# Performance work log

Hardware: AMD Instinct MI355X
Metric: run time of the kernel (lower is better)

Reference implementation:

```python
import jax, jax.numpy as jnp
import numpy as np


def setup_inputs() -> dict:
    key = jax.random.key(0)
    k1, k2, k3 = jax.random.split(key, 3)
    B, IN, H, OUT = 2048, 4096, 4096, 1024
    x = jax.random.normal(k1, (B, IN), dtype=jnp.float32)
    fc1_weight = jax.random.randint(k2, (H, IN), 0, 2).astype(jnp.int32)
    fc2_weight = jax.random.randint(k3, (OUT, H), 0, 2).astype(jnp.int32)
    return {"x": x, "fc1_weight": fc1_weight, "fc2_weight": fc2_weight, "threshold": 2048}


def _binary_popcount_matmul(a, w):
    # a: (B, K) in {0,1}, w: (N, K) in {0,1}
    # matches = sum_k 1 - (a XOR w) = a@w.T + (1-a)@(1-w).T  (identical math,
    # avoids materializing the (B, N, K) XNOR tensor the naive code builds)
    return jnp.einsum('bk,nk->bn', a, w) + jnp.einsum('bk,nk->bn', 1 - a, 1 - w)


def reference(x, fc1_weight, fc2_weight, threshold):
    xb = (x.reshape(x.shape[0], -1) >= 0).astype(jnp.int32)   # binarize input
    pc1 = _binary_popcount_matmul(xb, fc1_weight)              # (B, H) popcounts
    act1 = (pc1 >= threshold).astype(jnp.int32)                # threshold activation
    pc2 = _binary_popcount_matmul(act1, fc2_weight)            # (B, OUT) popcounts
    return pc2
```

## Files before the change

### kernel.cpp

```cpp
#include <hip/hip_runtime.h>
#include <stdint.h>

typedef int v4i  __attribute__((ext_vector_type(4)));
typedef int v16i __attribute__((ext_vector_type(16)));

__device__ __forceinline__ void gload_lds16(const void* g, void* l) {
    __builtin_amdgcn_global_load_lds(
        (const __attribute__((address_space(1))) void*)g,
        (__attribute__((address_space(3))) void*)l, 16, 0, 0);
}

template<typename T, bool ISFLOAT>
__global__ __launch_bounds__(512)
void pack_frag(const T* __restrict__ in, int8_t* __restrict__ F, int K) {
    __shared__ int8_t lbuf[32 * 528];
    const int t  = threadIdx.x;
    const int db = blockIdx.y;
    const int c0 = blockIdx.x << 9;

    #pragma unroll
    for (int p = 0; p < 8; ++p) {
        int idx = p * 512 + t;
        int row = idx >> 7, c4 = idx & 127;
        uint32_t b;
        if constexpr (ISFLOAT) {
            const float4 v = *(const float4*)(in + (size_t)(db * 32 + row) * K + c0 + c4 * 4);
            b =  (v.x >= 0.0f ? 0x01u : 0xFFu)
              | ((v.y >= 0.0f ? 0x01u : 0xFFu) << 8)
              | ((v.z >= 0.0f ? 0x01u : 0xFFu) << 16)
              | ((v.w >= 0.0f ? 0x01u : 0xFFu) << 24);
        } else {
            const int4 v = *(const int4*)(in + (size_t)(db * 32 + row) * K + c0 + c4 * 4);
            b =  (v.x ? 0x01u : 0xFFu)
              | ((v.y ? 0x01u : 0xFFu) << 8)
              | ((v.z ? 0x01u : 0xFFu) << 16)
              | ((v.w ? 0x01u : 0xFFu) << 24);
        }
        *(uint32_t*)(lbuf + row * 528 + c4 * 4) = b;
    }
    __syncthreads();

    const int s  = t >> 5;
    const int l0 = t & 31;
    const int KC = K >> 5;
    int8_t* dst = F + ((size_t)db * KC + (c0 >> 5) + s) * 1024;
    uint4 v0 = *(const uint4*)(lbuf + l0 * 528 + s * 32);
    uint4 v1 = *(const uint4*)(lbuf + l0 * 528 + s * 32 + 16);
    *(uint4*)(dst + l0 * 16) = v0;
    *(uint4*)(dst + (l0 + 32) * 16) = v1;
}

__global__ __launch_bounds__(512, 1)
void bnn_l1_opt(const int8_t* __restrict__ Af,
                const int8_t* __restrict__ Bf,
                const int* __restrict__ thr_ptr,
                int8_t* __restrict__ actf)
{
    constexpr int KC  = 128;
    constexpr int NKT = 64;
    constexpr uint32_t BUFSZ = 24576;

    __shared__ int8_t lds[4 * 24576];

    const int tid  = threadIdx.x;
    const int lane = tid & 63;
    const int wv   = tid >> 6;
    const int wr   = wv >> 2, wc = wv & 3;

    const int g   = blockIdx.x;
    const int idx = g >> 3;
    const int bn  = (g & 7) * 2 + (idx >> 4);
    const int bm  = idx & 15;

    const int8_t* gsrc[3];
    uint32_t loff[3];
    #pragma unroll
    for (int c = 0; c < 3; ++c) {
        int s = c * 512 + tid;
        if (s < 512) {
            int R = s >> 7, kk = (s >> 6) & 1, ln = s & 63;
            gsrc[c] = Af + ((size_t)(bm * 4 + R) * KC + kk) * 1024 + ln * 16;
            loff[c] = (uint32_t)s * 16;
        } else {
            int s2 = s - 512;
            int Cb = s2 >> 7, kk = (s2 >> 6) & 1, ln = s2 & 63;
            gsrc[c] = Bf + ((size_t)(bn * 8 + Cb) * KC + kk) * 1024 + ln * 16;
            loff[c] = 8192u + (uint32_t)s2 * 16;
        }
    }

    auto issue3 = [&](uint32_t bufo) {
        gload_lds16(gsrc[0], lds + bufo + loff[0]); gsrc[0] += 2048;
        gload_lds16(gsrc[1], lds + bufo + loff[1]); gsrc[1] += 2048;
        gload_lds16(gsrc[2], lds + bufo + loff[2]); gsrc[2] += 2048;
    };

    v16i acc[2][2];
    #pragma unroll
    for (int i = 0; i < 2; ++i)
        #pragma unroll
        for (int j = 0; j < 2; ++j) acc[i][j] = {};

    issue3(0);
    issue3(BUFSZ);
    issue3(2 * BUFSZ);

#define KT_BODY(KT, P)                                                         \
    {                                                                          \
        const int kt_ = (KT);                                                  \
        if (kt_ < NKT - 2)       asm volatile("s_waitcnt vmcnt(6)" ::: "memory"); \
        else if (kt_ == NKT - 2) asm volatile("s_waitcnt vmcnt(3)" ::: "memory"); \
        else                     asm volatile("s_waitcnt vmcnt(0)" ::: "memory"); \
        __builtin_amdgcn_sched_barrier(0);                                     \
        __builtin_amdgcn_s_barrier();                                          \
        __builtin_amdgcn_sched_barrier(0);                                     \
        const int8_t* Ab = lds + (P) * 24576 + wr * 4096 + lane * 16;          \
        const int8_t* Bb = lds + (P) * 24576 + 8192 + wc * 4096 + lane * 16;   \
        v4i a00 = *(const v4i*)(Ab + 0);                                       \
        v4i a01 = *(const v4i*)(Ab + 1024);                                    \
        v4i a10 = *(const v4i*)(Ab + 2048);                                    \
        v4i a11 = *(const v4i*)(Ab + 3072);                                    \
        v4i b00 = *(const v4i*)(Bb + 0);                                       \
        v4i b01 = *(const v4i*)(Bb + 1024);                                    \
        v4i b10 = *(const v4i*)(Bb + 2048);                                    \
        v4i b11 = *(const v4i*)(Bb + 3072);                                    \
        if (kt_ + 3 < NKT) issue3(((P) + 3) % 4 * 24576u);                     \
        __builtin_amdgcn_s_setprio(1);                                         \
        acc[0][0] = __builtin_amdgcn_mfma_i32_32x32x32_i8(a00, b00, acc[0][0], 0, 0, 0); \
        acc[0][1] = __builtin_amdgcn_mfma_i32_32x32x32_i8(a00, b10, acc[0][1], 0, 0, 0); \
        acc[1][0] = __builtin_amdgcn_mfma_i32_32x32x32_i8(a10, b00, acc[1][0], 0, 0, 0); \
        acc[1][1] = __builtin_amdgcn_mfma_i32_32x32x32_i8(a10, b10, acc[1][1], 0, 0, 0); \
        acc[0][0] = __builtin_amdgcn_mfma_i32_32x32x32_i8(a01, b01, acc[0][0], 0, 0, 0); \
        acc[0][1] = __builtin_amdgcn_mfma_i32_32x32x32_i8(a01, b11, acc[0][1], 0, 0, 0); \
        acc[1][0] = __builtin_amdgcn_mfma_i32_32x32x32_i8(a11, b01, acc[1][0], 0, 0, 0); \
        acc[1][1] = __builtin_amdgcn_mfma_i32_32x32x32_i8(a11, b11, acc[1][1], 0, 0, 0); \
        __builtin_amdgcn_s_setprio(0);                                         \
    }

    #pragma unroll 1
    for (int kt0 = 0; kt0 < NKT; kt0 += 4) {
        KT_BODY(kt0 + 0, 0)
        KT_BODY(kt0 + 1, 1)
        KT_BODY(kt0 + 2, 2)
        KT_BODY(kt0 + 3, 3)
    }
#undef KT_BODY

    __syncthreads();
    const int thr = *thr_ptr;
    int8_t* bits = lds;
    #pragma unroll
    for (int i = 0; i < 2; ++i)
        #pragma unroll
        for (int j = 0; j < 2; ++j) {
            int dimb = wr * 64 + i * 32 + 4 * (lane >> 5);
            int gcl  = wc * 64 + j * 32 + (lane & 31);
            #pragma unroll
            for (int reg = 0; reg < 16; ++reg) {
                int dl = dimb + (reg & 3) + 8 * (reg >> 2);
                int match = (4096 + acc[i][j][reg]) >> 1;
                bits[dl * 272 + gcl] = (match >= thr) ? (int8_t)1 : (int8_t)-1;
            }
        }
    __syncthreads();
    const int s    = tid >> 4;
    const int dblk = s >> 3, kcl = s & 7;
    const int l0   = (tid & 15) * 4;
    int8_t* dst = actf + ((size_t)(bm * 4 + dblk) * KC + bn * 8 + kcl) * 1024;
    #pragma unroll
    for (int li = 0; li < 4; ++li) {
        int l = l0 + li;
        uint4 v = *(const uint4*)(bits + (dblk * 32 + (l & 31)) * 272
                                       + kcl * 32 + (l >> 5) * 16);
        *(uint4*)(dst + l * 16) = v;
    }
}

template<int WN>
__global__ __launch_bounds__(256, 1)
void bnn_mfma2(const int8_t* __restrict__ Af,
               const int8_t* __restrict__ Bf,
               int* __restrict__ out, int Nout)
{
    constexpr int KC     = 128;
    constexpr int NKT    = 64;
    constexpr int NBB    = 2 * WN;
    constexpr int ASLOTS = 512;
    constexpr int BSLOTS = 128 * NBB;
    constexpr int SLOTS  = ASLOTS + BSLOTS;
    constexpr int NLD    = SLOTS / 256;
    constexpr uint32_t BUFSZ = (uint32_t)SLOTS * 16;

    __shared__ int8_t lds[3][SLOTS * 16];

    const int tid  = threadIdx.x;
    const int lane = tid & 63;
    const int wv   = tid >> 6;
    const int wr   = wv >> 1, wc = wv & 1;

    const int g   = blockIdx.x;
    const int idx = g >> 3;
    const int bn  = (g & 7) * 2 + (idx >> 4);
    const int bm  = idx & 15;

    const int8_t* gsrc[NLD];
    uint32_t ldoff[NLD];
    #pragma unroll
    for (int i = 0; i < NLD; ++i) {
        int sbase = wv * 64 + 256 * i;
        ldoff[i] = (uint32_t)sbase * 16;
        const int8_t* base;
        if (sbase < ASLOTS) {
            int R = sbase >> 7, C = (sbase >> 6) & 1;
            base = Af + ((size_t)(bm * 4 + R) * KC + C) * 1024;
        } else {
            int s = sbase - ASLOTS;
            int R = s >> 7, C = (s >> 6) & 1;
            base = Bf + ((size_t)(bn * NBB + R) * KC + C) * 1024;
        }
        gsrc[i] = base + lane * 16;
    }

    auto stage = [&](int buf) {
        #pragma unroll
        for (int i = 0; i < NLD; ++i) {
            gload_lds16(gsrc[i], (int8_t*)lds + (uint32_t)buf * BUFSZ + ldoff[i]);
            gsrc[i] += 2048;
        }
    };

    v16i acc[2][WN];
    #pragma unroll
    for (int i = 0; i < 2; ++i)
        #pragma unroll
        for (int j = 0; j < WN; ++j) acc[i][j] = {};

    stage(0);
    stage(1);

    int cur = 0, nxt = 2;
    #pragma unroll 1
    for (int kt = 0; kt < NKT; ++kt) {
        if (kt < NKT - 1) asm volatile("s_waitcnt vmcnt(3)" ::: "memory");
        else              asm volatile("s_waitcnt vmcnt(0)" ::: "memory");
        __builtin_amdgcn_sched_barrier(0);
        __builtin_amdgcn_s_barrier();
        __builtin_amdgcn_sched_barrier(0);

        if (kt < NKT - 2) {
            stage(nxt);
            nxt = (nxt == 2) ? 0 : nxt + 1;
        }

        const int8_t* Al = lds[cur];
        const int8_t* Bl = lds[cur] + ASLOTS * 16;
        #pragma unroll
        for (int kc = 0; kc < 2; ++kc) {
            v4i af[2], bf[WN];
            #pragma unroll
            for (int i = 0; i < 2; ++i)
                af[i] = *(const v4i*)(Al + (((wr * 2 + i) * 2 + kc) * 64 + lane) * 16);
            #pragma unroll
            for (int j = 0; j < WN; ++j)
                bf[j] = *(const v4i*)(Bl + (((wc * WN + j) * 2 + kc) * 64 + lane) * 16);
            #pragma unroll
            for (int i = 0; i < 2; ++i)
                #pragma unroll
                for (int j = 0; j < WN; ++j)
                    acc[i][j] = __builtin_amdgcn_mfma_i32_32x32x32_i8(af[i], bf[j], acc[i][j], 0, 0, 0);
        }
        cur = (cur == 2) ? 0 : cur + 1;
    }

    #pragma unroll
    for (int i = 0; i < 2; ++i)
        #pragma unroll
        for (int j = 0; j < WN; ++j) {
            int gc = bn * (64 * WN) + wc * (32 * WN) + j * 32 + (lane & 31);
            #pragma unroll
            for (int reg = 0; reg < 16; ++reg) {
                int gr = bm * 128 + wr * 64 + i * 32
                       + (reg & 3) + 8 * (reg >> 2) + 4 * (lane >> 5);
                out[(size_t)gr * Nout + gc] = (4096 + acc[i][j][reg]) >> 1;
            }
        }
}

extern "C" void kernel_launch(void* const* d_in, const int* in_sizes, int n_in,
                              void* d_out, int out_size, void* d_ws, size_t ws_size,
                              hipStream_t stream) {
    const float* x   = (const float*)d_in[0];
    const int*   w1  = (const int*)d_in[1];
    const int*   w2  = (const int*)d_in[2];
    const int*   thr = (const int*)d_in[3];
    int* out = (int*)d_out;

    const int B = 2048, IN = 4096, H = 4096, OUT = 1024;
    uint8_t* ws = (uint8_t*)d_ws;

    int8_t* Af  = (int8_t*)(ws);
    int8_t* W1f = (int8_t*)(ws + ((size_t)8  << 20));
    int8_t* W2f = (int8_t*)(ws + ((size_t)24 << 20));
    int8_t* Act = (int8_t*)(ws + ((size_t)28 << 20));

    pack_frag<float, true ><<<dim3(IN / 512, B   / 32), 512, 0, stream>>>(x,  Af,  IN);
    pack_frag<int,   false><<<dim3(IN / 512, H   / 32), 512, 0, stream>>>(w1, W1f, IN);
    pack_frag<int,   false><<<dim3(H  / 512, OUT / 32), 512, 0, stream>>>(w2, W2f, H);

    bnn_l1_opt<<<256, 512, 0, stream>>>(Af, W1f, thr, Act);
    bnn_mfma2<1><<<256, 256, 0, stream>>>(Act, W2f, out, OUT);
}
```

Before: 82.37 us.

## Merge pack kernels into one launch and retile layer-1 GEMM to 128x128 blocks

```diff
diff --git a/kernel.cpp b/kernel.cpp
--- a/kernel.cpp
+++ b/kernel.cpp
@@ -11,12 +11,13 @@
 }
 
 template<typename T, bool ISFLOAT>
-__global__ __launch_bounds__(512)
-void pack_frag(const T* __restrict__ in, int8_t* __restrict__ F, int K) {
+__device__ __forceinline__ void pack_block(const T* __restrict__ in,
+                                           int8_t* __restrict__ F,
+                                           int db, int strip) {
     __shared__ int8_t lbuf[32 * 528];
     const int t  = threadIdx.x;
-    const int db = blockIdx.y;
-    const int c0 = blockIdx.x << 9;
+    const int c0 = strip << 9;
+    constexpr int K = 4096, KC = 128;
 
     #pragma unroll
     for (int p = 0; p < 8; ++p) {
@@ -42,7 +43,6 @@
 
     const int s  = t >> 5;
     const int l0 = t & 31;
-    const int KC = K >> 5;
     int8_t* dst = F + ((size_t)db * KC + (c0 >> 5) + s) * 1024;
     uint4 v0 = *(const uint4*)(lbuf + l0 * 528 + s * 32);
     uint4 v1 = *(const uint4*)(lbuf + l0 * 528 + s * 32 + 16);
@@ -50,33 +50,49 @@
     *(uint4*)(dst + (l0 + 32) * 16) = v1;
 }
 
-__global__ __launch_bounds__(512, 1)
-void bnn_l1_opt(const int8_t* __restrict__ Af,
+__global__ __launch_bounds__(512)
+void pack_all(const float* __restrict__ x, const int* __restrict__ w1,
+              const int* __restrict__ w2, int8_t* __restrict__ Af,
+              int8_t* __restrict__ W1f, int8_t* __restrict__ W2f) {
+    int b = blockIdx.x;
+    if (b < 512) {
+        pack_block<float, true>(x, Af, b >> 3, b & 7);
+    } else if (b < 1536) {
+        int bb = b - 512;
+        pack_block<int, false>(w1, W1f, bb >> 3, bb & 7);
+    } else {
+        int bb = b - 1536;
+        pack_block<int, false>(w2, W2f, bb >> 3, bb & 7);
+    }
+}
+
+__global__ __launch_bounds__(256, 2)
+void bnn_l1_128(const int8_t* __restrict__ Af,
                 const int8_t* __restrict__ Bf,
                 const int* __restrict__ thr_ptr,
                 int8_t* __restrict__ actf)
 {
     constexpr int KC  = 128;
     constexpr int NKT = 64;
-    constexpr uint32_t BUFSZ = 24576;
-
-    __shared__ int8_t lds[4 * 24576];
+    constexpr uint32_t BUFSZ = 16384;
+
+    __shared__ int8_t lds[4 * 16384];
 
     const int tid  = threadIdx.x;
     const int lane = tid & 63;
     const int wv   = tid >> 6;
-    const int wr   = wv >> 2, wc = wv & 3;
+    const int wr   = wv >> 1, wc = wv & 1;
 
     const int g   = blockIdx.x;
     const int idx = g >> 3;
-    const int bn  = (g & 7) * 2 + (idx >> 4);
+    const int bn  = (g & 7) * 4 + (idx >> 4);
     const int bm  = idx & 15;
 
-    const int8_t* gsrc[3];
-    uint32_t loff[3];
-    #pragma unroll
-    for (int c = 0; c < 3; ++c) {
-        int s = c * 512 + tid;
+    const int8_t* gsrc[4];
+    uint32_t loff[4];
+    #pragma unroll
+    for (int c = 0; c < 4; ++c) {
+        int s = c * 256 + tid;
         if (s < 512) {
             int R = s >> 7, kk = (s >> 6) & 1, ln = s & 63;
             gsrc[c] = Af + ((size_t)(bm * 4 + R) * KC + kk) * 1024 + ln * 16;
@@ -84,15 +100,16 @@
         } else {
             int s2 = s - 512;
             int Cb = s2 >> 7, kk = (s2 >> 6) & 1, ln = s2 & 63;
-            gsrc[c] = Bf + ((size_t)(bn * 8 + Cb) * KC + kk) * 1024 + ln * 16;
+            gsrc[c] = Bf + ((size_t)(bn * 4 + Cb) * KC + kk) * 1024 + ln * 16;
             loff[c] = 8192u + (uint32_t)s2 * 16;
         }
     }
-
-    auto issue3 = [&](uint32_t bufo) {
-        gload_lds16(gsrc[0], lds + bufo + loff[0]); gsrc[0] += 2048;
-        gload_lds16(gsrc[1], lds + bufo + loff[1]); gsrc[1] += 2048;
-        gload_lds16(gsrc[2], lds + bufo + loff[2]); gsrc[2] += 2048;
+    auto issue4 = [&](uint32_t bufo) {
+        #pragma unroll
+        for (int c = 0; c < 4; ++c) {
+            gload_lds16(gsrc[c], lds + bufo + loff[c]);
+            gsrc[c] += 2048;
+        }
     };
 
     v16i acc[2][2];
@@ -101,21 +118,21 @@
         #pragma unroll
         for (int j = 0; j < 2; ++j) acc[i][j] = {};
 
-    issue3(0);
-    issue3(BUFSZ);
-    issue3(2 * BUFSZ);
+    issue4(0);
+    issue4(BUFSZ);
+    issue4(2 * BUFSZ);
 
 #define KT_BODY(KT, P)                                                         \
     {                                                                          \
         const int kt_ = (KT);                                                  \
-        if (kt_ < NKT - 2)       asm volatile("s_waitcnt vmcnt(6)" ::: "memory"); \
-        else if (kt_ == NKT - 2) asm volatile("s_waitcnt vmcnt(3)" ::: "memory"); \
+        if (kt_ < NKT - 2)       asm volatile("s_waitcnt vmcnt(8)" ::: "memory"); \
+        else if (kt_ == NKT - 2) asm volatile("s_waitcnt vmcnt(4)" ::: "memory"); \
         else                     asm volatile("s_waitcnt vmcnt(0)" ::: "memory"); \
         __builtin_amdgcn_sched_barrier(0);                                     \
         __builtin_amdgcn_s_barrier();                                          \
         __builtin_amdgcn_sched_barrier(0);                                     \
-        const int8_t* Ab = lds + (P) * 24576 + wr * 4096 + lane * 16;          \
-        const int8_t* Bb = lds + (P) * 24576 + 8192 + wc * 4096 + lane * 16;   \
+        const int8_t* Ab = lds + (P) * 16384 + wr * 4096 + lane * 16;          \
+        const int8_t* Bb = lds + (P) * 16384 + 8192 + wc * 4096 + lane * 16;   \
         v4i a00 = *(const v4i*)(Ab + 0);                                       \
         v4i a01 = *(const v4i*)(Ab + 1024);                                    \
         v4i a10 = *(const v4i*)(Ab + 2048);                                    \
@@ -124,7 +141,7 @@
         v4i b01 = *(const v4i*)(Bb + 1024);                                    \
         v4i b10 = *(const v4i*)(Bb + 2048);                                    \
         v4i b11 = *(const v4i*)(Bb + 3072);                                    \
-        if (kt_ + 3 < NKT) issue3(((P) + 3) % 4 * 24576u);                     \
+        if (kt_ + 3 < NKT) issue4((uint32_t)(((P) + 3) & 3) * 16384u);         \
         __builtin_amdgcn_s_setprio(1);                                         \
         acc[0][0] = __builtin_amdgcn_mfma_i32_32x32x32_i8(a00, b00, acc[0][0], 0, 0, 0); \
         acc[0][1] = __builtin_amdgcn_mfma_i32_32x32x32_i8(a00, b10, acc[0][1], 0, 0, 0); \
@@ -159,18 +176,18 @@
             for (int reg = 0; reg < 16; ++reg) {
                 int dl = dimb + (reg & 3) + 8 * (reg >> 2);
                 int match = (4096 + acc[i][j][reg]) >> 1;
-                bits[dl * 272 + gcl] = (match >= thr) ? (int8_t)1 : (int8_t)-1;
+                bits[dl * 144 + gcl] = (match >= thr) ? (int8_t)1 : (int8_t)-1;
             }
         }
     __syncthreads();
     const int s    = tid >> 4;
-    const int dblk = s >> 3, kcl = s & 7;
+    const int dblk = s >> 2, kcl = s & 3;
     const int l0   = (tid & 15) * 4;
-    int8_t* dst = actf + ((size_t)(bm * 4 + dblk) * KC + bn * 8 + kcl) * 1024;
+    int8_t* dst = actf + ((size_t)(bm * 4 + dblk) * KC + bn * 4 + kcl) * 1024;
     #pragma unroll
     for (int li = 0; li < 4; ++li) {
         int l = l0 + li;
-        uint4 v = *(const uint4*)(bits + (dblk * 32 + (l & 31)) * 272
+        uint4 v = *(const uint4*)(bits + (dblk * 32 + (l & 31)) * 144
                                        + kcl * 32 + (l >> 5) * 16);
         *(uint4*)(dst + l * 16) = v;
     }
@@ -295,7 +312,7 @@
     const int*   thr = (const int*)d_in[3];
     int* out = (int*)d_out;
 
-    const int B = 2048, IN = 4096, H = 4096, OUT = 1024;
+    const int OUT = 1024;
     uint8_t* ws = (uint8_t*)d_ws;
 
     int8_t* Af  = (int8_t*)(ws);
@@ -303,10 +320,7 @@
     int8_t* W2f = (int8_t*)(ws + ((size_t)24 << 20));
     int8_t* Act = (int8_t*)(ws + ((size_t)28 << 20));
 
-    pack_frag<float, true ><<<dim3(IN / 512, B   / 32), 512, 0, stream>>>(x,  Af,  IN);
-    pack_frag<int,   false><<<dim3(IN / 512, H   / 32), 512, 0, stream>>>(w1, W1f, IN);
-    pack_frag<int,   false><<<dim3(H  / 512, OUT / 32), 512, 0, stream>>>(w2, W2f, H);
-
-    bnn_l1_opt<<<256, 512, 0, stream>>>(Af, W1f, thr, Act);
+    pack_all<<<1792, 512, 0, stream>>>(x, w1, w2, Af, W1f, W2f);
+    bnn_l1_128<<<512, 256, 0, stream>>>(Af, W1f, thr, Act);
     bnn_mfma2<1><<<256, 256, 0, stream>>>(Act, W2f, out, OUT);
 }
```

After: 77.88 us. -5.4%, faster.
